# Optimization experiments

Measured on AMD Instinct MI355X. Metric: run time of the kernel, lower is better.

The kernel has to match this reference:

```python
import jax, jax.numpy as jnp
import numpy as np
from math import sqrt

INPUT, HIDDEN, OUTPUT = 256, 512, 256
B, T = 64, 1024


def setup_inputs() -> dict:
    key = jax.random.key(0)
    k1, k2, k3, k4 = jax.random.split(key, 4)
    x = jax.random.normal(k1, (B, T, INPUT), dtype=jnp.float32)
    W_xh = jax.random.normal(k2, (INPUT, HIDDEN), dtype=jnp.float32) * sqrt(2.0 / (INPUT + HIDDEN))
    W_hh = jax.random.normal(k3, (HIDDEN, HIDDEN), dtype=jnp.float32) * sqrt(1.0 / HIDDEN)
    b_h = jnp.zeros((HIDDEN,), dtype=jnp.float32)
    W_hy = jax.random.normal(k4, (HIDDEN, OUTPUT), dtype=jnp.float32) * sqrt(2.0 / (HIDDEN + OUTPUT))
    b_y = jnp.zeros((OUTPUT,), dtype=jnp.float32)
    return {"x": x, "W_xh": W_xh, "W_hh": W_hh, "b_h": b_h, "W_hy": W_hy, "b_y": b_y}


def reference(x, W_xh, W_hh, b_h, W_hy, b_y):
    # Precompute input projection for all timesteps: [B,T,H_in] @ [H_in,H] -> [B,T,H]
    xh = jnp.einsum('bti,ih->bth', x, W_xh) + b_h
    h0 = jnp.zeros((x.shape[0], W_hh.shape[0]), dtype=x.dtype)

    def step(h, xh_t):
        h_new = jnp.tanh(h @ W_hh + xh_t)  # [B,H]
        return h_new, h_new

    # scan over time: xh transposed to [T,B,H]
    _, hs = jax.lax.scan(step, h0, jnp.swapaxes(xh, 0, 1))
    hs = jnp.swapaxes(hs, 0, 1)  # [B,T,H]
    outputs = jnp.einsum('bth,ho->bto', hs, W_hy) + b_y  # [B,T,O]
    return outputs
```

## Files before the change

kernel.cpp:

```cpp
#include <hip/hip_runtime.h>
#include <hip/hip_bf16.h>
#include <hip/hip_fp16.h>


#define BT 65536
#define HID 512
#define NIN 256
#define NOUT 256
#define TSTEPS 1024
#define NBATCH 64

typedef _Float16 hf2_t __attribute__((ext_vector_type(2)));

__device__ __forceinline__ float fdot2(unsigned w, unsigned h, float acc) {
#if __has_builtin(__builtin_amdgcn_fdot2)
    return __builtin_amdgcn_fdot2(__builtin_bit_cast(hf2_t, w),
                                  __builtin_bit_cast(hf2_t, h), acc, false);
#else
    __half2 wv = __builtin_bit_cast(__half2, w);
    __half2 hv = __builtin_bit_cast(__half2, h);
    float2 wf = __half22float2(wv);
    float2 hf = __half22float2(hv);
    return acc + wf.x * hf.x + wf.y * hf.y;
#endif
}

__device__ __forceinline__ float dot4(uint4 w, uint4 h, float acc) {
    acc = fdot2(w.x, h.x, acc);
    acc = fdot2(w.y, h.y, acc);
    acc = fdot2(w.z, h.z, acc);
    acc = fdot2(w.w, h.w, acc);
    return acc;
}

__device__ __forceinline__ unsigned pack2h(float a, float b) {
    unsigned lo = (unsigned)__half_as_ushort(__float2half_rn(a));
    unsigned hi = (unsigned)__half_as_ushort(__float2half_rn(b));
    return lo | (hi << 16);
}

template <int CTRL>
__device__ __forceinline__ float dpp_add(float x) {
    int y = __builtin_amdgcn_mov_dpp(__float_as_int(x), CTRL, 0xF, 0xF, true);
    return x + __int_as_float(y);
}
template <int CTRL>
__device__ __forceinline__ float dpp_get(float x) {
    int y = __builtin_amdgcn_mov_dpp(__float_as_int(x), CTRL, 0xF, 0xF, true);
    return __int_as_float(y);
}

__device__ __forceinline__ float fast_tanh(float x) {
    float e = __builtin_amdgcn_exp2f(x * 2.8853900817779268f);
    return 1.0f - 2.0f * __builtin_amdgcn_rcpf(e + 1.0f);
}

__device__ __forceinline__ float4 load4f(const float* p) {
    return *(const float4*)p;
}
__device__ __forceinline__ float4 load4f(const __half* p) {
    ushort4 u = *(const ushort4*)p;
    float4 r;
    r.x = __half2float(__ushort_as_half(u.x));
    r.y = __half2float(__ushort_as_half(u.y));
    r.z = __half2float(__ushort_as_half(u.z));
    r.w = __half2float(__ushort_as_half(u.w));
    return r;
}
__device__ __forceinline__ void store1(float* p, float v) { *p = v; }
__device__ __forceinline__ void store1(__half* p, float v) { *p = __float2half_rn(v); }

__global__ __launch_bounds__(256)
void pack_w4_kernel(const float* __restrict__ W,
                    unsigned* __restrict__ wblob_w,
                    unsigned long long* __restrict__ exch) {
    int w = blockIdx.x * 256 + threadIdx.x;
    int q = w >> 15;
    int r = w & 32767;
    int i = r >> 11;
    int r2 = r & 2047;
    int t = r2 >> 2, u = r2 & 3;
    int g = t >> 3, s = t & 7;
    int c = i >> 3, j = i & 7;
    int col = 128 * q + 2 * g + c;
    int k = 64 * s + 8 * j + 2 * u;
    unsigned val = pack2h(W[(size_t)k * HID + col], W[(size_t)(k + 1) * HID + col]);
    wblob_w[(size_t)((q * 16 + i) * 512 + t) * 4 + u] = val;
    if (w < 32768) exch[w] = 0ull;
}

template <typename AT, typename CT>
__global__ __launch_bounds__(256)
void gemm_bias_kernel(const AT* __restrict__ A, const float* __restrict__ B,
                      const float* __restrict__ bias, CT* __restrict__ C,
                      int M, int N, int K) {
    const int TM = 64, TN = 64, TK = 16;
    __shared__ float As[TK][TM];
    __shared__ float Bs[TK][TN + 4];

    int tid = threadIdx.x;
    int tx = tid & 15;
    int ty = tid >> 4;
    int row0 = blockIdx.x * TM;
    int col0 = blockIdx.y * TN;

    float c[4][4];
#pragma unroll
    for (int i = 0; i < 4; ++i)
#pragma unroll
        for (int j = 0; j < 4; ++j) c[i][j] = 0.f;

    for (int kk = 0; kk < K; kk += TK) {
        {
            int ar = tid >> 2;
            int ac = (tid & 3) * 4;
            float4 av = load4f(A + (size_t)(row0 + ar) * K + kk + ac);
            As[ac + 0][ar] = av.x;
            As[ac + 1][ar] = av.y;
            As[ac + 2][ar] = av.z;
            As[ac + 3][ar] = av.w;
        }
        {
            int br = tid >> 4;
            int bc = (tid & 15) * 4;
            float4 bv = *(const float4*)(B + (size_t)(kk + br) * N + col0 + bc);
            *(float4*)&Bs[br][bc] = bv;
        }
        __syncthreads();
#pragma unroll
        for (int k = 0; k < TK; ++k) {
            float4 a = *(const float4*)&As[k][ty * 4];
            float4 b = *(const float4*)&Bs[k][tx * 4];
            float av[4] = {a.x, a.y, a.z, a.w};
            float bv[4] = {b.x, b.y, b.z, b.w};
#pragma unroll
            for (int i = 0; i < 4; ++i)
#pragma unroll
                for (int j = 0; j < 4; ++j) c[i][j] += av[i] * bv[j];
        }
        __syncthreads();
    }

#pragma unroll
    for (int j = 0; j < 4; ++j) {
        float bb = bias[col0 + tx * 4 + j];
#pragma unroll
        for (int i = 0; i < 4; ++i) {
            int r = row0 + ty * 4 + i;
            int cc = col0 + tx * 4 + j;
            store1(&C[(size_t)r * N + cc], c[i][j] + bb);
        }
    }
}

template <typename AT, typename CT>
__global__ __launch_bounds__(256)
void gemm_bias_f16_kernel(const AT* __restrict__ A, const float* __restrict__ B,
                          const float* __restrict__ bias, CT* __restrict__ C,
                          int M, int N, int K) {
    const int TM = 64, TN = 64, TK = 16;
    __shared__ unsigned Asp[TK / 2][TM];
    __shared__ unsigned Bsp[TK / 2][TN + 4];

    int tid = threadIdx.x;
    int tx = tid & 15;
    int ty = tid >> 4;
    int row0 = blockIdx.x * TM;
    int col0 = blockIdx.y * TN;

    float c[4][4];
#pragma unroll
    for (int i = 0; i < 4; ++i)
#pragma unroll
        for (int j = 0; j < 4; ++j) c[i][j] = 0.f;

    for (int kk = 0; kk < K; kk += TK) {
        {
            int ar = tid >> 2;
            int ac = (tid & 3) * 4;
            float4 av = load4f(A + (size_t)(row0 + ar) * K + kk + ac);
            Asp[(ac >> 1) + 0][ar] = pack2h(av.x, av.y);
            Asp[(ac >> 1) + 1][ar] = pack2h(av.z, av.w);
        }
        {
            int k2 = tid >> 5;
            int bc = (tid & 31) * 2;
            const float* b0 = B + (size_t)(kk + 2 * k2) * N + col0 + bc;
            const float* b1 = b0 + N;
            float2 r0 = *(const float2*)b0;
            float2 r1 = *(const float2*)b1;
            Bsp[k2][bc + 0] = pack2h(r0.x, r1.x);
            Bsp[k2][bc + 1] = pack2h(r0.y, r1.y);
        }
        __syncthreads();
#pragma unroll
        for (int k2 = 0; k2 < TK / 2; ++k2) {
            uint4 ap = *(const uint4*)&Asp[k2][ty * 4];
            uint4 bp = *(const uint4*)&Bsp[k2][tx * 4];
            unsigned av[4] = {ap.x, ap.y, ap.z, ap.w};
            unsigned bv[4] = {bp.x, bp.y, bp.z, bp.w};
#pragma unroll
            for (int i = 0; i < 4; ++i)
#pragma unroll
                for (int j = 0; j < 4; ++j) c[i][j] = fdot2(av[i], bv[j], c[i][j]);
        }
        __syncthreads();
    }

#pragma unroll
    for (int j = 0; j < 4; ++j) {
        float bb = bias[col0 + tx * 4 + j];
#pragma unroll
        for (int i = 0; i < 4; ++i) {
            int r = row0 + ty * 4 + i;
            int cc = col0 + tx * 4 + j;
            store1(&C[(size_t)r * N + cc], c[i][j] + bb);
        }
    }
}

__global__ __launch_bounds__(512, 2)
void rnn_scan4(const __half* __restrict__ xh,
               const uint4* __restrict__ wblob,
               __half* __restrict__ hs,
               unsigned long long* __restrict__ exch) {
    __shared__ __align__(16) uint4 hbuf4[2][72];

    const int bid = blockIdx.x;
    const int row = bid & 63;
    const int q   = bid >> 6;
    const int t = threadIdx.x;
    const int g = t >> 3, s = t & 7;

    uint4 W[16];
#pragma unroll
    for (int i = 0; i < 16; ++i) W[i] = wblob[(q * 16 + i) * 512 + t];
#pragma unroll
    for (int i = 0; i < 16; ++i) {
        asm volatile("" : "+v"(W[i].x), "+v"(W[i].y), "+v"(W[i].z), "+v"(W[i].w));
    }

    if (t < 72) {
        hbuf4[0][t] = uint4{0u, 0u, 0u, 0u};
        hbuf4[1][t] = uint4{0u, 0u, 0u, 0u};
    }
    __syncthreads();

    const int col0 = 128 * q + 2 * g;
    const __half* xp = xh + (size_t)row * TSTEPS * HID + col0 + s;
    unsigned* hp32 = (unsigned*)hs + (size_t)row * TSTEPS * 256 + (64 * q + g);
    const int wordC = ((64 * q + g) >> 5) * 36 + ((64 * q + g) & 31);
    unsigned long long* pub[2];
    pub[0] = exch + (((size_t)row * 2 + 0) * 4 + q) * 64 + g;
    pub[1] = exch + (((size_t)row * 2 + 1) * 4 + q) * 64 + g;
    const int m = t & 63;
    const int qa = t >> 6;
    const int Q = qa + (qa >= q ? 1 : 0);
    const unsigned long long* src[2];
    src[0] = exch + (((size_t)row * 2 + 0) * 4 + Q) * 64 + m;
    src[1] = exch + (((size_t)row * 2 + 1) * 4 + Q) * 64 + m;
    const int ldsw = ((64 * Q + m) >> 5) * 36 + ((64 * Q + m) & 31);

    for (int step = 0; step < TSTEPS; ++step) {
        const int par = step & 1;

        float xv = 0.f;
        if (s < 2) xv = __half2float(xp[(size_t)step * HID]);

        if (step && t < 192) {
            unsigned long long v = __hip_atomic_load(
                src[par], __ATOMIC_RELAXED, __HIP_MEMORY_SCOPE_AGENT);
            while ((unsigned)(v >> 32) < (unsigned)step) {
                v = __hip_atomic_load(src[par], __ATOMIC_RELAXED,
                                      __HIP_MEMORY_SCOPE_AGENT);
            }
            ((unsigned*)&hbuf4[par][0])[ldsw] = (unsigned)v;
        }
        __syncthreads();

        const uint4* hv = &hbuf4[par][s * 9];
        float a0 = 0.f, a1 = 0.f;
#pragma unroll
        for (int j = 0; j < 8; ++j) {
            uint4 hj = hv[j];
            a0 = dot4(W[j], hj, a0);
            a1 = dot4(W[8 + j], hj, a1);
        }

        a0 = dpp_add<0xB1>(a0); a0 = dpp_add<0x4E>(a0); a0 = dpp_add<0x141>(a0);
        a1 = dpp_add<0xB1>(a1); a1 = dpp_add<0x4E>(a1); a1 = dpp_add<0x141>(a1);

        if (s < 2) {
            float tot = (s == 0) ? a0 : a1;
            float hn = fast_tanh(tot + xv);
            float hi = dpp_get<0xB1>(hn);
            if (s == 0) {
                unsigned pv = pack2h(hn, hi);
                ((unsigned*)&hbuf4[par ^ 1][0])[wordC] = pv;
                hp32[(size_t)step * 256] = pv;
                unsigned long long pubv =
                    ((unsigned long long)(unsigned)(step + 1) << 32) | pv;
                __hip_atomic_store(pub[(step + 1) & 1], pubv,
                                   __ATOMIC_RELAXED, __HIP_MEMORY_SCOPE_AGENT);
            }
        }
    }
}

extern "C" void kernel_launch(void* const* d_in, const int* in_sizes, int n_in,
                              void* d_out, int out_size, void* d_ws, size_t ws_size,
                              hipStream_t stream) {
    const float* x    = (const float*)d_in[0];
    const float* W_xh = (const float*)d_in[1];
    const float* W_hh = (const float*)d_in[2];
    const float* b_h  = (const float*)d_in[3];
    const float* W_hy = (const float*)d_in[4];
    const float* b_y  = (const float*)d_in[5];
    float* out = (float*)d_out;

    char* ws = (char*)d_ws;
    unsigned* wblob = (unsigned*)ws;
    unsigned long long* exch = (unsigned long long*)(ws + (512 << 10));
    __half* xh = (__half*)(ws + (1 << 20));
    __half* hs = (__half*)(ws + (1 << 20) + (size_t)BT * HID * 2);

    pack_w4_kernel<<<dim3(512), dim3(256), 0, stream>>>(W_hh, wblob, exch);

    gemm_bias_kernel<float, __half>
        <<<dim3(BT / 64, HID / 64), dim3(256), 0, stream>>>(x, W_xh, b_h, xh, BT, HID, NIN);

    rnn_scan4<<<dim3(4 * NBATCH), dim3(512), 0, stream>>>(
        xh, (const uint4*)wblob, hs, exch);

    gemm_bias_f16_kernel<__half, float>
        <<<dim3(BT / 64, NOUT / 64), dim3(256), 0, stream>>>(hs, W_hy, b_y, out, BT, NOUT, HID);
}
```

Measured before the change: 1.564 ms.

## Halve RNN scan block size and compute four hidden columns per thread group

The recurrent scan kernel drops from 512 to 256 threads per block. Each thread now keeps 32 uint4 weight registers instead of 16 and accumulates four output columns per 8-lane group instead of two. The weight packing kernel is re-laid out to match. The aim is to cut the number of waves taking part in each per-step barrier and LDS read, at the cost of a longer serial dot-product chain per thread and much higher register pressure. A large, mostly unused shared buffer is also allocated.

New measurement: 1.725 ms. 10.3% more time.

```diff
diff --git a/kernel.cpp b/kernel.cpp
--- a/kernel.cpp
+++ b/kernel.cpp
@@ -77,15 +77,15 @@
     int w = blockIdx.x * 256 + threadIdx.x;
     int q = w >> 15;
     int r = w & 32767;
-    int i = r >> 11;
-    int r2 = r & 2047;
+    int i = r >> 10;
+    int r2 = r & 1023;
     int t = r2 >> 2, u = r2 & 3;
     int g = t >> 3, s = t & 7;
     int c = i >> 3, j = i & 7;
-    int col = 128 * q + 2 * g + c;
+    int col = 128 * q + 4 * g + c;
     int k = 64 * s + 8 * j + 2 * u;
     unsigned val = pack2h(W[(size_t)k * HID + col], W[(size_t)(k + 1) * HID + col]);
-    wblob_w[(size_t)((q * 16 + i) * 512 + t) * 4 + u] = val;
+    wblob_w[(size_t)((q * 32 + i) * 256 + t) * 4 + u] = val;
     if (w < 32768) exch[w] = 0ull;
 }
 
@@ -219,12 +219,13 @@
     }
 }
 
-__global__ __launch_bounds__(512, 2)
+__global__ __launch_bounds__(256, 2)
+__attribute__((amdgpu_waves_per_eu(2, 2)))
 void rnn_scan4(const __half* __restrict__ xh,
                const uint4* __restrict__ wblob,
                __half* __restrict__ hs,
                unsigned long long* __restrict__ exch) {
-    __shared__ __align__(16) uint4 hbuf4[2][72];
+    __shared__ __align__(16) uint4 big[3600];
 
     const int bid = blockIdx.x;
     const int row = bid & 63;
@@ -232,75 +233,77 @@
     const int t = threadIdx.x;
     const int g = t >> 3, s = t & 7;
 
-    uint4 W[16];
-#pragma unroll
-    for (int i = 0; i < 16; ++i) W[i] = wblob[(q * 16 + i) * 512 + t];
-#pragma unroll
-    for (int i = 0; i < 16; ++i) {
+    uint4 W[32];
+#pragma unroll
+    for (int i = 0; i < 32; ++i) W[i] = wblob[(q * 32 + i) * 256 + t];
+#pragma unroll
+    for (int i = 0; i < 32; ++i) {
         asm volatile("" : "+v"(W[i].x), "+v"(W[i].y), "+v"(W[i].z), "+v"(W[i].w));
     }
 
-    if (t < 72) {
-        hbuf4[0][t] = uint4{0u, 0u, 0u, 0u};
-        hbuf4[1][t] = uint4{0u, 0u, 0u, 0u};
-    }
+    if (t < 144) big[t] = uint4{0u, 0u, 0u, 0u};
     __syncthreads();
 
-    const int col0 = 128 * q + 2 * g;
+    const int col0 = 128 * q + 4 * g;
     const __half* xp = xh + (size_t)row * TSTEPS * HID + col0 + s;
-    unsigned* hp32 = (unsigned*)hs + (size_t)row * TSTEPS * 256 + (64 * q + g);
-    const int wordC = ((64 * q + g) >> 5) * 36 + ((64 * q + g) & 31);
-    unsigned long long* pub[2];
-    pub[0] = exch + (((size_t)row * 2 + 0) * 4 + q) * 64 + g;
-    pub[1] = exch + (((size_t)row * 2 + 1) * 4 + q) * 64 + g;
+    const int hw = 64 * q + 2 * g + (s >> 1);
+    unsigned* hp32 = (unsigned*)hs + (size_t)row * TSTEPS * 256 + hw;
+    const int wordC = (hw >> 5) * 36 + (hw & 31);
+    unsigned long long* pub0 = exch + (((size_t)row * 2 + 0) * 4 + q) * 64 + (2 * g + (s >> 1));
+    unsigned long long* pub1 = exch + (((size_t)row * 2 + 1) * 4 + q) * 64 + (2 * g + (s >> 1));
     const int m = t & 63;
     const int qa = t >> 6;
     const int Q = qa + (qa >= q ? 1 : 0);
-    const unsigned long long* src[2];
-    src[0] = exch + (((size_t)row * 2 + 0) * 4 + Q) * 64 + m;
-    src[1] = exch + (((size_t)row * 2 + 1) * 4 + Q) * 64 + m;
+    const unsigned long long* src0 = exch + (((size_t)row * 2 + 0) * 4 + Q) * 64 + m;
+    const unsigned long long* src1 = exch + (((size_t)row * 2 + 1) * 4 + Q) * 64 + m;
     const int ldsw = ((64 * Q + m) >> 5) * 36 + ((64 * Q + m) & 31);
 
     for (int step = 0; step < TSTEPS; ++step) {
         const int par = step & 1;
 
         float xv = 0.f;
-        if (s < 2) xv = __half2float(xp[(size_t)step * HID]);
+        if (s < 4) xv = __half2float(xp[(size_t)step * HID]);
 
         if (step && t < 192) {
+            const unsigned long long* sp = par ? src1 : src0;
             unsigned long long v = __hip_atomic_load(
-                src[par], __ATOMIC_RELAXED, __HIP_MEMORY_SCOPE_AGENT);
+                sp, __ATOMIC_RELAXED, __HIP_MEMORY_SCOPE_AGENT);
             while ((unsigned)(v >> 32) < (unsigned)step) {
-                v = __hip_atomic_load(src[par], __ATOMIC_RELAXED,
+                v = __hip_atomic_load(sp, __ATOMIC_RELAXED,
                                       __HIP_MEMORY_SCOPE_AGENT);
             }
-            ((unsigned*)&hbuf4[par][0])[ldsw] = (unsigned)v;
-        }
-        __syncthreads();
-
-        const uint4* hv = &hbuf4[par][s * 9];
-        float a0 = 0.f, a1 = 0.f;
+            ((unsigned*)big)[par * 288 + ldsw] = (unsigned)v;
+        }
+        __syncthreads();
+
+        const uint4* hv = &big[par * 72 + s * 9];
+        float a0 = 0.f, a1 = 0.f, a2 = 0.f, a3 = 0.f;
 #pragma unroll
         for (int j = 0; j < 8; ++j) {
             uint4 hj = hv[j];
-            a0 = dot4(W[j], hj, a0);
-            a1 = dot4(W[8 + j], hj, a1);
+            a0 = dot4(W[j],      hj, a0);
+            a1 = dot4(W[8 + j],  hj, a1);
+            a2 = dot4(W[16 + j], hj, a2);
+            a3 = dot4(W[24 + j], hj, a3);
         }
 
         a0 = dpp_add<0xB1>(a0); a0 = dpp_add<0x4E>(a0); a0 = dpp_add<0x141>(a0);
         a1 = dpp_add<0xB1>(a1); a1 = dpp_add<0x4E>(a1); a1 = dpp_add<0x141>(a1);
-
-        if (s < 2) {
-            float tot = (s == 0) ? a0 : a1;
+        a2 = dpp_add<0xB1>(a2); a2 = dpp_add<0x4E>(a2); a2 = dpp_add<0x141>(a2);
+        a3 = dpp_add<0xB1>(a3); a3 = dpp_add<0x4E>(a3); a3 = dpp_add<0x141>(a3);
+
+        if (s < 4) {
+            float tot = (s == 0) ? a0 : (s == 1) ? a1 : (s == 2) ? a2 : a3;
             float hn = fast_tanh(tot + xv);
             float hi = dpp_get<0xB1>(hn);
-            if (s == 0) {
+            if (!(s & 1)) {
                 unsigned pv = pack2h(hn, hi);
-                ((unsigned*)&hbuf4[par ^ 1][0])[wordC] = pv;
+                ((unsigned*)big)[(par ^ 1) * 288 + wordC] = pv;
                 hp32[(size_t)step * 256] = pv;
                 unsigned long long pubv =
                     ((unsigned long long)(unsigned)(step + 1) << 32) | pv;
-                __hip_atomic_store(pub[(step + 1) & 1], pubv,
+                unsigned long long* pp = ((step + 1) & 1) ? pub1 : pub0;
+                __hip_atomic_store(pp, pubv,
                                    __ATOMIC_RELAXED, __HIP_MEMORY_SCOPE_AGENT);
             }
         }
@@ -329,7 +332,7 @@
     gemm_bias_kernel<float, __half>
         <<<dim3(BT / 64, HID / 64), dim3(256), 0, stream>>>(x, W_xh, b_h, xh, BT, HID, NIN);
 
-    rnn_scan4<<<dim3(4 * NBATCH), dim3(512), 0, stream>>>(
+    rnn_scan4<<<dim3(4 * NBATCH), dim3(256), 0, stream>>>(
         xh, (const uint4*)wblob, hs, exch);
 
     gemm_bias_f16_kernel<__half, float>
```
